# Performance work log

Measured on AMD Instinct MI355X. Metric: run time of the kernel, lower is better.

## Reference

```python
import jax, jax.numpy as jnp
import numpy as np

B, N, T, D, H, E = 2, 1024, 8, 128, 4, 8192
DH = D // H
NEG_SLOPE = 0.2  # GATv2Conv default negative_slope


def _ln(x, g, b):
    m = jnp.mean(x, -1, keepdims=True)
    v = jnp.mean((x - m) ** 2, -1, keepdims=True)
    return (x - m) * jax.lax.rsqrt(v + 1e-5) * g + b


def _forward(x, edge_index, gat_wl, gat_wr, gat_att, gat_b, in_w, in_b, out_w, out_b,
             ffn_w1, ffn_b1, ffn_w2, ffn_b2, fus_w, fus_b,
             lns_g, lns_b, lnt1_g, lnt1_b, lnt2_g, lnt2_b, lnf_g, lnf_b):
    # ---- spatial branch: GATv2, vectorized over (B, T) instead of python loops ----
    loops = jnp.arange(N)
    src = jnp.concatenate([edge_index[0], loops])  # j: message source (PyG adds self loops)
    dst = jnp.concatenate([edge_index[1], loops])  # i: aggregation target
    xl = jnp.einsum('bntd,de->bnte', x, gat_wl).reshape(B, N, T, H, D)
    xr = jnp.einsum('bntd,de->bnte', x, gat_wr).reshape(B, N, T, H, D)
    ml = xl[:, src]                                  # [B,Et,T,H,D]
    mr = xr[:, dst]
    e = jax.nn.leaky_relu(ml + mr, NEG_SLOPE)
    logits = jnp.einsum('bethd,hd->beth', e, gat_att)
    logits = jnp.moveaxis(logits, 1, 0)              # [Et,B,T,H]
    mx = jax.ops.segment_max(logits, dst, num_segments=N)
    p = jnp.exp(logits - mx[dst])                    # stable edge softmax per dst node
    ssum = jax.ops.segment_sum(p, dst, num_segments=N)
    alpha = p / ssum[dst]                            # [Et,B,T,H]
    msg = alpha[..., None] * jnp.moveaxis(ml, 1, 0)
    agg = jax.ops.segment_sum(msg, dst, num_segments=N)  # [N,B,T,H,D]
    x_sp = jnp.moveaxis(agg.mean(3), 0, 1) + gat_b   # concat=False -> head mean; [B,N,T,D]
    x_sp = _ln(x_sp, lns_g, lns_b)

    # ---- temporal branch: MHA + FFN, vectorized over all B*N nodes ----
    xt = x.reshape(B * N, T, D)
    qkv = xt @ in_w + in_b
    q, k, v = jnp.split(qkv, 3, axis=-1)
    q = q.reshape(B * N, T, H, DH)
    k = k.reshape(B * N, T, H, DH)
    v = v.reshape(B * N, T, H, DH)
    scores = jnp.einsum('bthd,bshd->bhts', q, k) / np.float32(np.sqrt(DH))
    attn = jax.nn.softmax(scores, -1)
    o = jnp.einsum('bhts,bshd->bthd', attn, v).reshape(B * N, T, D)
    o = o @ out_w + out_b
    x1 = _ln(xt + o, lnt1_g, lnt1_b)
    ffn = jax.nn.gelu(x1 @ ffn_w1 + ffn_b1, approximate=False) @ ffn_w2 + ffn_b2
    x_tp = _ln(x1 + ffn, lnt2_g, lnt2_b).reshape(B, N, T, D)

    # ---- gated fusion with residual ----
    g = jax.nn.sigmoid(jnp.concatenate([x_sp, x_tp], -1) @ fus_w + fus_b)
    return _ln(g * x_sp + (1.0 - g) * x_tp + x, lnf_g, lnf_b)


def setup_inputs() -> dict:
    key = jax.random.key(0)
    ks = jax.random.split(key, 12)
    s = 0.05
    f = jnp.float32
    return {
        'x': jax.random.normal(ks[0], (B, N, T, D), f),
        'edge_index': jax.random.randint(ks[1], (2, E), 0, N),
        'gat_wl': jax.random.normal(ks[2], (D, H * D), f) * s,
        'gat_wr': jax.random.normal(ks[3], (D, H * D), f) * s,
        'gat_att': jax.random.normal(ks[4], (H, D), f) * s,
        'gat_b': jnp.zeros((D,), f),
        'in_w': jax.random.normal(ks[5], (D, 3 * D), f) * s,
        'in_b': jnp.zeros((3 * D,), f),
        'out_w': jax.random.normal(ks[6], (D, D), f) * s,
        'out_b': jnp.zeros((D,), f),
        'ffn_w1': jax.random.normal(ks[7], (D, 4 * D), f) * s,
        'ffn_b1': jnp.zeros((4 * D,), f),
        'ffn_w2': jax.random.normal(ks[8], (4 * D, D), f) * s,
        'ffn_b2': jnp.zeros((D,), f),
        'fus_w': jax.random.normal(ks[9], (2 * D, D), f) * s,
        'fus_b': jnp.zeros((D,), f),
        'lns_g': jnp.ones((D,), f), 'lns_b': jnp.zeros((D,), f),
        'lnt1_g': jnp.ones((D,), f), 'lnt1_b': jnp.zeros((D,), f),
        'lnt2_g': jnp.ones((D,), f), 'lnt2_b': jnp.zeros((D,), f),
        'lnf_g': jnp.ones((D,), f), 'lnf_b': jnp.zeros((D,), f),
    }


def reference(x, edge_index, gat_wl, gat_wr, gat_att, gat_b, in_w, in_b, out_w, out_b,
              ffn_w1, ffn_b1, ffn_w2, ffn_b2, fus_w, fus_b,
              lns_g, lns_b, lnt1_g, lnt1_b, lnt2_g, lnt2_b, lnf_g, lnf_b):
    return _forward(x, edge_index, gat_wl, gat_wr, gat_att, gat_b, in_w, in_b, out_w, out_b,
                    ffn_w1, ffn_b1, ffn_w2, ffn_b2, fus_w, fus_b,
                    lns_g, lns_b, lnt1_g, lnt1_b, lnt2_g, lnt2_b, lnf_g, lnf_b)
```

## Files before the change

### kernel.cpp

```cpp
#include <hip/hip_runtime.h>
#include <math.h>

#define B_ 2
#define N_ 1024
#define T_ 8
#define D_ 128
#define H_ 4
#define E_ 8192
#define EN_ 9216
#define M_ 16384

typedef unsigned short u16;
using bf16x8 = __attribute__((ext_vector_type(8))) short;
using f32x4  = __attribute__((ext_vector_type(4))) float;

__device__ __forceinline__ float bf2f(unsigned int u) {
  return __uint_as_float(u << 16);
}
__device__ __forceinline__ u16 f2bf(float f) {
  unsigned int x = __float_as_uint(f);
  x += 0x7fffu + ((x >> 16) & 1u);
  return (u16)(x >> 16);
}
__device__ __forceinline__ void load8f(const u16* p, float* f) {
  uint4 u = *(const uint4*)p;
  f[0]=bf2f(u.x & 0xffffu); f[1]=bf2f(u.x >> 16);
  f[2]=bf2f(u.y & 0xffffu); f[3]=bf2f(u.y >> 16);
  f[4]=bf2f(u.z & 0xffffu); f[5]=bf2f(u.z >> 16);
  f[6]=bf2f(u.w & 0xffffu); f[7]=bf2f(u.w >> 16);
}
__device__ __forceinline__ void unpack8(uint4 u, float* f) {
  f[0]=bf2f(u.x & 0xffffu); f[1]=bf2f(u.x >> 16);
  f[2]=bf2f(u.y & 0xffffu); f[3]=bf2f(u.y >> 16);
  f[4]=bf2f(u.z & 0xffffu); f[5]=bf2f(u.z >> 16);
  f[6]=bf2f(u.w & 0xffffu); f[7]=bf2f(u.w >> 16);
}
__device__ __forceinline__ void gl2lds(const u16* g, u16* l) {
  __builtin_amdgcn_global_load_lds(
      (const __attribute__((address_space(1))) unsigned int*)(const void*)g,
      (__attribute__((address_space(3))) unsigned int*)(void*)l,
      16, 0, 0);
}

__device__ __forceinline__ size_t bt_row(int r) {
  return (size_t)(((r >> 13) << 3) | (r & 7)) * 1024 + ((r >> 3) & 1023);
}

__device__ __forceinline__ u16 conv_w_elem(int idx,
    const float* wl, const float* wr, const float* inw, const float* outw,
    const float* f1, const float* f2, const float* fw) {
  const float* src; int base, K, N;
  if      (idx < 65536)  { src = wl;   base = 0;      K = 128; N = 512; }
  else if (idx < 131072) { src = wr;   base = 65536;  K = 128; N = 512; }
  else if (idx < 180224) { src = inw;  base = 131072; K = 128; N = 384; }
  else if (idx < 196608) { src = outw; base = 180224; K = 128; N = 128; }
  else if (idx < 262144) { src = f1;   base = 196608; K = 128; N = 512; }
  else if (idx < 327680) { src = f2;   base = 262144; K = 512; N = 128; }
  else                   { src = fw;   base = 327680; K = 256; N = 128; }
  int o = idx - base;
  int n = o / K, k = o - n * K;
  return f2bf(src[k * N + n]);
}

__global__ __launch_bounds__(1024) void prep_csr_k(const float* __restrict__ x,
    const float* __restrict__ wl, const float* __restrict__ wr,
    const float* __restrict__ inw, const float* __restrict__ outw,
    const float* __restrict__ f1, const float* __restrict__ f2,
    const float* __restrict__ fw,
    u16* __restrict__ XB, u16* __restrict__ WB,
    const int* __restrict__ ei, int* __restrict__ offs, int* __restrict__ srcs) {
  __shared__ int cnt[N_];
  __shared__ int cur[N_];
  int bi = blockIdx.x;
  int tid = threadIdx.x;
  if (bi < 512) {
    int i = (bi * 1024 + tid) * 4;
    float4 v = *(const float4*)&x[i];
    u16 o[4] = {f2bf(v.x), f2bf(v.y), f2bf(v.z), f2bf(v.w)};
    *(ushort4*)&XB[i] = *(ushort4*)o;
    return;
  }
  if (bi < 600) {
    int base = (bi - 512) * 4096 + tid * 4;
#pragma unroll
    for (int j = 0; j < 4; ++j)
      WB[base + j] = conv_w_elem(base + j, wl, wr, inw, outw, f1, f2, fw);
    return;
  }
  cnt[tid] = 0;
  __syncthreads();
  for (int e = tid; e < EN_; e += 1024) {
    int d = (e < E_) ? ei[E_ + e] : (e - E_);
    atomicAdd(&cnt[d], 1);
  }
  __syncthreads();
  int mine = cnt[tid];
  for (int off = 1; off < 1024; off <<= 1) {
    int tv = (tid >= off) ? cnt[tid - off] : 0;
    __syncthreads();
    cnt[tid] += tv;
    __syncthreads();
  }
  int excl = cnt[tid] - mine;
  offs[tid] = excl;
  if (tid == 1023) offs[N_] = cnt[1023];
  cur[tid] = excl;
  __syncthreads();
  for (int e = tid; e < EN_; e += 1024) {
    int d = (e < E_) ? ei[E_ + e] : (e - E_);
    int s = (e < E_) ? ei[e] : (e - E_);
    int pos = atomicAdd(&cur[d], 1);
    srcs[pos] = s;
  }
}

__global__ __launch_bounds__(256) void proj_k(const u16* __restrict__ XB,
    const u16* __restrict__ WT1, const float* __restrict__ in_b,
    u16* __restrict__ XL, u16* __restrict__ XR, u16* __restrict__ QKV) {
  __shared__ u16 As[128 * 128];
  __shared__ u16 Bs[128 * 128];
  int bx = blockIdx.x, by = blockIdx.y;
  int tid = threadIdx.x;
  int lane = tid & 63, wid = tid >> 6;
  int lr = lane & 15, lk = lane >> 4;
  int wm = (wid >> 1) * 64, wn = (wid & 1) * 64;

#pragma unroll
  for (int kc = 0; kc < 4; ++kc) {
#pragma unroll
    for (int i = 0; i < 2; ++i) {
      int o = tid * 16 + i * 4096;
      int row = o >> 6;
      int col = (o >> 1) & 31;
      gl2lds(XB + (size_t)(by * 128 + row) * 128 + kc * 32 + col,
             (u16*)((char*)As + kc * 8192 + i * 4096 + wid * 1024));
      gl2lds(WT1 + (size_t)(bx * 128 + row) * 128 + kc * 32 + col,
             (u16*)((char*)Bs + kc * 8192 + i * 4096 + wid * 1024));
    }
  }
  __syncthreads();

  f32x4 acc[4][4] = {};
#pragma unroll
  for (int kc = 0; kc < 4; ++kc) {
    bf16x8 bf[4];
#pragma unroll
    for (int ni = 0; ni < 4; ++ni)
      bf[ni] = *(const bf16x8*)&Bs[kc * 4096 + (wn + ni * 16 + lr) * 32 + lk * 8];
#pragma unroll
    for (int mi = 0; mi < 4; ++mi) {
      bf16x8 af = *(const bf16x8*)&As[kc * 4096 + (wm + mi * 16 + lr) * 32 + lk * 8];
#pragma unroll
      for (int ni = 0; ni < 4; ++ni)
        acc[mi][ni] = __builtin_amdgcn_mfma_f32_16x16x32_bf16(af, bf[ni], acc[mi][ni], 0, 0, 0);
    }
  }

  u16* Cb; int ldc_; int col0; const float* bias_; int remap;
  if (bx < 4)      { Cb = XL;  ldc_ = 512; col0 = bx * 128;       bias_ = nullptr; remap = 1; }
  else if (bx < 8) { Cb = XR;  ldc_ = 512; col0 = (bx - 4) * 128; bias_ = nullptr; remap = 1; }
  else             { Cb = QKV; ldc_ = 384; col0 = (bx - 8) * 128; bias_ = in_b;    remap = 0; }
  float bc[4];
#pragma unroll
  for (int ni = 0; ni < 4; ++ni)
    bc[ni] = bias_ ? bias_[col0 + wn + ni * 16 + lr] : 0.f;

  __syncthreads();
#pragma unroll
  for (int mi = 0; mi < 4; ++mi) {
#pragma unroll
    for (int r = 0; r < 4; ++r) {
      int rowl = wm + mi * 16 + lk * 4 + r;
#pragma unroll
      for (int ni = 0; ni < 4; ++ni) {
        int col = wn + ni * 16 + lr;
        As[rowl * 128 + (col ^ ((rowl & 7) << 3))] = f2bf(acc[mi][ni][r] + bc[ni]);
      }
    }
  }
  __syncthreads();
  {
    int chunk = tid & 15;
    int rbase = tid >> 4;
#pragma unroll
    for (int pass = 0; pass < 8; ++pass) {
      int rowl = pass * 16 + rbase;
      int row = by * 128 + rowl;
      size_t orow = remap ? bt_row(row) : (size_t)row;
      int sw = (chunk ^ (rowl & 7)) * 8;
      *(uint4*)&Cb[orow * ldc_ + col0 + chunk * 8] =
          *(const uint4*)&As[rowl * 128 + sw];
    }
  }
}

__global__ __launch_bounds__(256) void gat_k(const u16* __restrict__ XL,
    const u16* __restrict__ XR,
    const int* __restrict__ offs, const int* __restrict__ srcs,
    const float* __restrict__ att, const float* __restrict__ gb,
    const float* __restrict__ lng, const float* __restrict__ lnb,
    u16* __restrict__ XCAT) {
  int bid = blockIdx.x;
  int lane = threadIdx.x & 63;
  int wid = threadIdx.x >> 6;
  int xcd = bid & 7;
  int slot = bid >> 3;
  int p = ((slot >> 8) << 3) | xcd;
  int n = (slot & 255) * 4 + wid;
  int b = p >> 3, t = p & 7;
  int dd = (lane & 15) * 8;
  size_t tokn = (size_t)(b * N_ + n) * 8 + t;
  const u16* XLs = XL + (size_t)p * 1024 * 512;

  float mr[8], av[8];
  load8f(XR + ((size_t)p * 1024 + n) * 512 + lane * 8, mr);
  *(float4*)&av[0] = *(const float4*)(att + lane * 8);
  *(float4*)&av[4] = *(const float4*)(att + lane * 8 + 4);

  int beg = offs[n], end = offs[n + 1];
  float sH = 0.f;
  float acc[8] = {0.f, 0.f, 0.f, 0.f, 0.f, 0.f, 0.f, 0.f};
  int i = beg;
  uint4 r0 = *(const uint4*)(XLs + (size_t)srcs[i] * 512 + lane * 8);
  uint4 r1 = r0;
  if (i + 1 < end)
    r1 = *(const uint4*)(XLs + (size_t)srcs[i + 1] * 512 + lane * 8);
  while (i + 1 < end) {
    uint4 c0 = r0, c1 = r1;
    if (i + 2 < end)
      r0 = *(const uint4*)(XLs + (size_t)srcs[i + 2] * 512 + lane * 8);
    if (i + 3 < end)
      r1 = *(const uint4*)(XLs + (size_t)srcs[i + 3] * 512 + lane * 8);
    float ml0[8], ml1[8];
    unpack8(c0, ml0);
    unpack8(c1, ml1);
    float d0 = 0.f, d1 = 0.f;
#pragma unroll
    for (int j = 0; j < 8; ++j) {
      float m0 = ml0[j] + mr[j];
      m0 = fmaxf(m0, 0.2f * m0);
      d0 += m0 * av[j];
      float m1 = ml1[j] + mr[j];
      m1 = fmaxf(m1, 0.2f * m1);
      d1 += m1 * av[j];
    }
    d0 += __shfl_xor(d0, 1, 64); d1 += __shfl_xor(d1, 1, 64);
    d0 += __shfl_xor(d0, 2, 64); d1 += __shfl_xor(d1, 2, 64);
    d0 += __shfl_xor(d0, 4, 64); d1 += __shfl_xor(d1, 4, 64);
    d0 += __shfl_xor(d0, 8, 64); d1 += __shfl_xor(d1, 8, 64);
    float p0 = __expf(d0), p1 = __expf(d1);
    sH += p0 + p1;
#pragma unroll
    for (int j = 0; j < 8; ++j) acc[j] += p0 * ml0[j] + p1 * ml1[j];
    i += 2;
  }
  if (i < end) {
    float ml0[8];
    unpack8(r0, ml0);
    float d0 = 0.f;
#pragma unroll
    for (int j = 0; j < 8; ++j) {
      float m0 = ml0[j] + mr[j];
      m0 = fmaxf(m0, 0.2f * m0);
      d0 += m0 * av[j];
    }
    d0 += __shfl_xor(d0, 1, 64);
    d0 += __shfl_xor(d0, 2, 64);
    d0 += __shfl_xor(d0, 4, 64);
    d0 += __shfl_xor(d0, 8, 64);
    float p0 = __expf(d0);
    sH += p0;
#pragma unroll
    for (int j = 0; j < 8; ++j) acc[j] += p0 * ml0[j];
  }
  float invS = 1.f / sH;
#pragma unroll
  for (int j = 0; j < 8; ++j) acc[j] *= invS;
#pragma unroll
  for (int j = 0; j < 8; ++j) {
    acc[j] += __shfl_xor(acc[j], 16, 64);
    acc[j] += __shfl_xor(acc[j], 32, 64);
  }
#pragma unroll
  for (int j = 0; j < 8; ++j) acc[j] = acc[j] * 0.25f + gb[dd + j];
  float s = 0.f, s2 = 0.f;
#pragma unroll
  for (int j = 0; j < 8; ++j) { s += acc[j]; s2 += acc[j] * acc[j]; }
#pragma unroll
  for (int m = 1; m < 16; m <<= 1) {
    s += __shfl_xor(s, m, 64);
    s2 += __shfl_xor(s2, m, 64);
  }
  float mean = s * (1.f / 128.f);
  float var = s2 * (1.f / 128.f) - mean * mean;
  float r = rsqrtf(var + 1e-5f);
  if (lane < 16) {
    u16 ob[8];
#pragma unroll
    for (int j = 0; j < 8; ++j)
      ob[j] = f2bf((acc[j] - mean) * r * lng[dd + j] + lnb[dd + j]);
    *(uint4*)&XCAT[tokn * 256 + dd] = *(uint4*)ob;
  }
}

__global__ __launch_bounds__(256) void tower_k(const u16* __restrict__ QKV,
    const u16* __restrict__ WTO, const float* __restrict__ out_b,
    const float* __restrict__ x,
    const float* __restrict__ lnt1_g, const float* __restrict__ lnt1_b,
    const u16* __restrict__ WTF1, const u16* __restrict__ WTF2,
    const float* __restrict__ b1, const float* __restrict__ b2,
    const float* __restrict__ lnt2_g, const float* __restrict__ lnt2_b,
    u16* __restrict__ XCATr) {
  __shared__ u16 P[4 * 32 * 32];
  __shared__ u16 Wb[16384];
  __shared__ u16 Hc[2 * 32 * 40];
  __shared__ float rs[64], rq[64];
  int by = blockIdx.x;
  int tid = threadIdx.x;
  int lane = tid & 63, wid = tid >> 6;
  int lr = lane & 15, lk = lane >> 4;
  int wm = (wid >> 1) * 16, wn = (wid & 1) * 64;

#pragma unroll
  for (int i = 0; i < 8; ++i) {
    int o = tid * 16 + i * 4096;
    int c = o >> 13;
    int wb = o & 8191;
    int nrow = wb >> 6;
    int kin = (wb & 63) >> 1;
    gl2lds(WTO + (size_t)nrow * 128 + c * 32 + kin,
           (u16*)((char*)Wb + wid * 1024 + i * 4096));
  }
  int t = lane >> 3, sidx = lane & 7, dg = lane & 7;
  for (int it = 0; it < 4; ++it) {
    int task = wid * 4 + it;
    int bnl = task >> 2, h = task & 3;
    int bn = by * 4 + bnl;
    const u16* base = QKV + (size_t)bn * 8 * 384;
    float va[8][4];
#pragma unroll
    for (int s2 = 0; s2 < 8; ++s2) {
      ushort4 vv = *(const ushort4*)(base + s2 * 384 + 256 + h * 32 + dg * 4);
      va[s2][0] = bf2f(vv.x); va[s2][1] = bf2f(vv.y);
      va[s2][2] = bf2f(vv.z); va[s2][3] = bf2f(vv.w);
    }
    const u16* qp = base + t * 384 + h * 32;
    const u16* kp = base + sidx * 384 + 128 + h * 32;
    float sc = 0.f;
#pragma unroll
    for (int d0 = 0; d0 < 32; d0 += 8) {
      float q[8], k[8];
      load8f(qp + d0, q);
      load8f(kp + d0, k);
#pragma unroll
      for (int j = 0; j < 8; ++j) sc += q[j] * k[j];
    }
    sc *= 0.17677669529663687f;
    float m = sc;
    m = fmaxf(m, __shfl_xor(m, 1, 64));
    m = fmaxf(m, __shfl_xor(m, 2, 64));
    m = fmaxf(m, __shfl_xor(m, 4, 64));
    float p = __expf(sc - m);
    float S = p;
    S += __shfl_xor(S, 1, 64);
    S += __shfl_xor(S, 2, 64);
    S += __shfl_xor(S, 4, 64);
    float alpha = p / S;
    int tb = lane & 56;
    float o0 = 0.f, o1 = 0.f, o2 = 0.f, o3 = 0.f;
#pragma unroll
    for (int s2 = 0; s2 < 8; ++s2) {
      float a = __shfl(alpha, tb + s2, 64);
      o0 += a * va[s2][0];
      o1 += a * va[s2][1];
      o2 += a * va[s2][2];
      o3 += a * va[s2][3];
    }
    u16 ov[4] = {f2bf(o0), f2bf(o1), f2bf(o2), f2bf(o3)};
    int row = bnl * 8 + t;
    *(ushort4*)&P[h * 1024 + row * 32 + dg * 4] = *(ushort4*)ov;
  }
  __syncthreads();

  f32x4 acc[4] = {};
#pragma unroll
  for (int c = 0; c < 4; ++c) {
    bf16x8 bf[4];
#pragma unroll
    for (int ni = 0; ni < 4; ++ni)
      bf[ni] = *(const bf16x8*)&Wb[c * 4096 + (wn + ni * 16 + lr) * 32 + lk * 8];
    bf16x8 af = *(const bf16x8*)&P[c * 1024 + (wm + lr) * 32 + lk * 8];
#pragma unroll
    for (int ni = 0; ni < 4; ++ni)
      acc[ni] = __builtin_amdgcn_mfma_f32_16x16x32_bf16(af, bf[ni], acc[ni], 0, 0, 0);
  }

  f32x4 x1r[4];
  {
    float bc[4];
#pragma unroll
    for (int ni = 0; ni < 4; ++ni) bc[ni] = out_b[wn + ni * 16 + lr];
#pragma unroll
    for (int r = 0; r < 4; ++r) {
      int rowl = wm + lk * 4 + r;
      int row = by * 32 + rowl;
      float s = 0.f, s2 = 0.f;
#pragma unroll
      for (int ni = 0; ni < 4; ++ni) {
        int col = wn + ni * 16 + lr;
        float v = acc[ni][r] + bc[ni] + x[(size_t)row * 128 + col];
        acc[ni][r] = v;
        s += v; s2 += v * v;
      }
      s += __shfl_xor(s, 1, 64); s2 += __shfl_xor(s2, 1, 64);
      s += __shfl_xor(s, 2, 64); s2 += __shfl_xor(s2, 2, 64);
      s += __shfl_xor(s, 4, 64); s2 += __shfl_xor(s2, 4, 64);
      s += __shfl_xor(s, 8, 64); s2 += __shfl_xor(s2, 8, 64);
      if (lr == 0) {
        rs[rowl * 2 + (wid & 1)] = s;
        rq[rowl * 2 + (wid & 1)] = s2;
      }
    }
    __syncthreads();
#pragma unroll
    for (int r = 0; r < 4; ++r) {
      int rowl = wm + lk * 4 + r;
      float tot = rs[rowl * 2] + rs[rowl * 2 + 1];
      float tq = rq[rowl * 2] + rq[rowl * 2 + 1];
      float mean = tot * (1.f / 128.f);
      float var = tq * (1.f / 128.f) - mean * mean;
      float rinv = rsqrtf(var + 1e-5f);
#pragma unroll
      for (int ni = 0; ni < 4; ++ni) {
        int col = wn + ni * 16 + lr;
        float o = (acc[ni][r] - mean) * rinv * lnt1_g[col] + lnt1_b[col];
        x1r[ni][r] = o;
        P[(col >> 5) * 1024 + rowl * 32 + (col & 31)] = f2bf(o);
      }
    }
  }

  int wr0 = (wid >> 1) * 16, wc0 = (wid & 1) * 32;
  f32x4 acc2[4] = {};
  for (int nc = 0; nc < 8; ++nc) {
    __syncthreads();
#pragma unroll
    for (int kc = 0; kc < 4; ++kc) {
      gl2lds(WTF1 + (size_t)(nc * 64 + (tid >> 2)) * 128 + kc * 32 + (tid & 3) * 8,
             (u16*)((char*)Wb + kc * 4096 + wid * 1024));
    }
#pragma unroll
    for (int i = 0; i < 4; ++i) {
      int o = tid * 16 + i * 4096;
      int kc2l = o >> 13;
      int wb = o & 8191;
      int nrow = wb >> 6;
      int kin = (wb & 63) >> 1;
      gl2lds(WTF2 + (size_t)nrow * 512 + nc * 64 + kc2l * 32 + kin,
             (u16*)((char*)Wb + 16384 + wid * 1024 + i * 4096));
    }
    __syncthreads();
    f32x4 a1[2] = {};
#pragma unroll
    for (int kc = 0; kc < 4; ++kc) {
      bf16x8 bf0 = *(const bf16x8*)&Wb[kc * 2048 + (wc0 + lr) * 32 + lk * 8];
      bf16x8 bf1 = *(const bf16x8*)&Wb[kc * 2048 + (wc0 + 16 + lr) * 32 + lk * 8];
      bf16x8 af = *(const bf16x8*)&P[kc * 1024 + (wr0 + lr) * 32 + lk * 8];
      a1[0] = __builtin_amdgcn_mfma_f32_16x16x32_bf16(af, bf0, a1[0], 0, 0, 0);
      a1[1] = __builtin_amdgcn_mfma_f32_16x16x32_bf16(af, bf1, a1[1], 0, 0, 0);
    }
#pragma unroll
    for (int r = 0; r < 4; ++r) {
      int row = wr0 + lk * 4 + r;
#pragma unroll
      for (int ni = 0; ni < 2; ++ni) {
        int cl = wc0 + ni * 16 + lr;
        float v = a1[ni][r] + b1[nc * 64 + cl];
        v = 0.5f * v * (1.f + erff(v * 0.70710678118f));
        Hc[(cl >> 5) * 1280 + row * 40 + (cl & 31)] = f2bf(v);
      }
    }
    __syncthreads();
#pragma unroll
    for (int kc2l = 0; kc2l < 2; ++kc2l) {
      bf16x8 bf[4];
#pragma unroll
      for (int ni = 0; ni < 4; ++ni)
        bf[ni] = *(const bf16x8*)&Wb[8192 + kc2l * 4096 + (wn + ni * 16 + lr) * 32 + lk * 8];
      bf16x8 af = *(const bf16x8*)&Hc[kc2l * 1280 + (wm + lr) * 40 + lk * 8];
#pragma unroll
      for (int ni = 0; ni < 4; ++ni)
        acc2[ni] = __builtin_amdgcn_mfma_f32_16x16x32_bf16(af, bf[ni], acc2[ni], 0, 0, 0);
    }
  }
  __syncthreads();

  {
    float bc[4];
#pragma unroll
    for (int ni = 0; ni < 4; ++ni) bc[ni] = b2[wn + ni * 16 + lr];
#pragma unroll
    for (int r = 0; r < 4; ++r) {
      int rowl = wm + lk * 4 + r;
      float s = 0.f, s2 = 0.f;
#pragma unroll
      for (int ni = 0; ni < 4; ++ni) {
        float v = acc2[ni][r] + bc[ni] + x1r[ni][r];
        acc2[ni][r] = v;
        s += v; s2 += v * v;
      }
      s += __shfl_xor(s, 1, 64); s2 += __shfl_xor(s2, 1, 64);
      s += __shfl_xor(s, 2, 64); s2 += __shfl_xor(s2, 2, 64);
      s += __shfl_xor(s, 4, 64); s2 += __shfl_xor(s2, 4, 64);
      s += __shfl_xor(s, 8, 64); s2 += __shfl_xor(s2, 8, 64);
      if (lr == 0) {
        rs[rowl * 2 + (wid & 1)] = s;
        rq[rowl * 2 + (wid & 1)] = s2;
      }
    }
    __syncthreads();
#pragma unroll
    for (int r = 0; r < 4; ++r) {
      int rowl = wm + lk * 4 + r;
      float tot = rs[rowl * 2] + rs[rowl * 2 + 1];
      float tq = rq[rowl * 2] + rq[rowl * 2 + 1];
      float mean = tot * (1.f / 128.f);
      float var = tq * (1.f / 128.f) - mean * mean;
      float rinv = rsqrtf(var + 1e-5f);
#pragma unroll
      for (int ni = 0; ni < 4; ++ni) {
        int col = wn + ni * 16 + lr;
        float o = (acc2[ni][r] - mean) * rinv * lnt2_g[col] + lnt2_b[col];
        P[rowl * 128 + (col ^ ((rowl & 7) << 3))] = f2bf(o);
      }
    }
    __syncthreads();
    {
      int chunk = tid & 15;
      int rbase = tid >> 4;
#pragma unroll
      for (int pass = 0; pass < 2; ++pass) {
        int rowl = pass * 16 + rbase;
        int sw = (chunk ^ (rowl & 7)) * 8;
        *(uint4*)&XCATr[(size_t)(by * 32 + rowl) * 256 + chunk * 8] =
            *(const uint4*)&P[rowl * 128 + sw];
      }
    }
  }
}

__global__ __launch_bounds__(256) void fusion_k(const u16* __restrict__ A,
    const u16* __restrict__ WT, const float* __restrict__ bias,
    const float* __restrict__ xres, const u16* __restrict__ xcat,
    const float* __restrict__ lng, const float* __restrict__ lnb,
    float* __restrict__ o32) {
  __shared__ u16 As[32 * 32];
  __shared__ u16 Bs[128 * 32];
  __shared__ float rs[64], rq[64];
  int by = blockIdx.x;
  int tid = threadIdx.x;
  int lane = tid & 63, wid = tid >> 6;
  int lr = lane & 15, lk = lane >> 4;
  int wm = (wid >> 1) * 16, wn = (wid & 1) * 64;
  const int K = 256;

  f32x4 acc[4] = {};
  for (int k0 = 0; k0 < K; k0 += 32) {
    __syncthreads();
    if (tid < 128) {
      int o = tid * 16;
      gl2lds(A + (size_t)(by * 32 + (o >> 6)) * K + k0 + ((o >> 1) & 31),
             (u16*)((char*)As + wid * 1024));
    }
#pragma unroll
    for (int i = 0; i < 2; ++i) {
      int o = tid * 16 + i * 4096;
      gl2lds(WT + (size_t)(o >> 6) * K + k0 + ((o >> 1) & 31),
             (u16*)((char*)Bs + wid * 1024 + i * 4096));
    }
    __syncthreads();
    bf16x8 bf[4];
#pragma unroll
    for (int ni = 0; ni < 4; ++ni)
      bf[ni] = *(const bf16x8*)&Bs[(wn + ni * 16 + lr) * 32 + lk * 8];
    bf16x8 af = *(const bf16x8*)&As[(wm + lr) * 32 + lk * 8];
#pragma unroll
    for (int ni = 0; ni < 4; ++ni)
      acc[ni] = __builtin_amdgcn_mfma_f32_16x16x32_bf16(af, bf[ni], acc[ni], 0, 0, 0);
  }
  float bc[4];
#pragma unroll
  for (int ni = 0; ni < 4; ++ni) bc[ni] = bias[wn + ni * 16 + lr];
#pragma unroll
  for (int r = 0; r < 4; ++r) {
    int rowl = wm + lk * 4 + r;
    int row = by * 32 + rowl;
    float s = 0.f, s2 = 0.f;
#pragma unroll
    for (int ni = 0; ni < 4; ++ni) {
      int col = wn + ni * 16 + lr;
      float v = acc[ni][r] + bc[ni];
      float gg = 1.f / (1.f + __expf(-v));
      float xsp = bf2f(xcat[(size_t)row * 256 + col]);
      float xtp = bf2f(xcat[(size_t)row * 256 + 128 + col]);
      v = gg * xsp + (1.f - gg) * xtp + xres[(size_t)row * 128 + col];
      acc[ni][r] = v;
      s += v; s2 += v * v;
    }
    s += __shfl_xor(s, 1, 64); s2 += __shfl_xor(s2, 1, 64);
    s += __shfl_xor(s, 2, 64); s2 += __shfl_xor(s2, 2, 64);
    s += __shfl_xor(s, 4, 64); s2 += __shfl_xor(s2, 4, 64);
    s += __shfl_xor(s, 8, 64); s2 += __shfl_xor(s2, 8, 64);
    if (lr == 0) {
      rs[rowl * 2 + (wid & 1)] = s;
      rq[rowl * 2 + (wid & 1)] = s2;
    }
  }
  __syncthreads();
#pragma unroll
  for (int r = 0; r < 4; ++r) {
    int rowl = wm + lk * 4 + r;
    int row = by * 32 + rowl;
    float tot = rs[rowl * 2] + rs[rowl * 2 + 1];
    float tq = rq[rowl * 2] + rq[rowl * 2 + 1];
    float mean = tot * (1.f / 128.f);
    float var = tq * (1.f / 128.f) - mean * mean;
    float rinv = rsqrtf(var + 1e-5f);
#pragma unroll
    for (int ni = 0; ni < 4; ++ni) {
      int col = wn + ni * 16 + lr;
      o32[(size_t)row * 128 + col] =
          (acc[ni][r] - mean) * rinv * lng[col] + lnb[col];
    }
  }
}

extern "C" void kernel_launch(void* const* d_in, const int* in_sizes, int n_in,
                              void* d_out, int out_size, void* d_ws, size_t ws_size,
                              hipStream_t stream) {
  const float* x       = (const float*)d_in[0];
  const int*   ei      = (const int*)d_in[1];
  const float* gat_att = (const float*)d_in[4];
  const float* gat_b   = (const float*)d_in[5];
  const float* in_b    = (const float*)d_in[7];
  const float* out_b   = (const float*)d_in[9];
  const float* ffn_b1  = (const float*)d_in[11];
  const float* ffn_b2  = (const float*)d_in[13];
  const float* fus_b   = (const float*)d_in[15];
  const float* lns_g   = (const float*)d_in[16];
  const float* lns_b   = (const float*)d_in[17];
  const float* lnt1_g  = (const float*)d_in[18];
  const float* lnt1_b  = (const float*)d_in[19];
  const float* lnt2_g  = (const float*)d_in[20];
  const float* lnt2_b  = (const float*)d_in[21];
  const float* lnf_g   = (const float*)d_in[22];
  const float* lnf_b   = (const float*)d_in[23];

  char* ws = (char*)d_ws;
  u16*   WB    = (u16*)ws;
  u16*   WTO   = WB + 180224;
  u16*   WTF1  = WB + 196608;
  u16*   WTF2  = WB + 262144;
  u16*   WTFUS = WB + 327680;
  int*   OFFS  = (int*)(ws + 3145728);
  int*   SRCS  = (int*)(ws + 3153920);
  u16*   XB   = (u16*)(ws + 4194304);
  u16*   XL   = (u16*)(ws + 8388608);
  u16*   XR   = (u16*)(ws + 25165824);
  u16*   QKV  = (u16*)(ws + 50331648);
  u16*   XCAT = (u16*)(ws + 67108864);

  prep_csr_k<<<dim3(601), dim3(1024), 0, stream>>>(x,
      (const float*)d_in[2], (const float*)d_in[3], (const float*)d_in[6],
      (const float*)d_in[8], (const float*)d_in[10], (const float*)d_in[12],
      (const float*)d_in[14], XB, WB, ei, OFFS, SRCS);

  proj_k<<<dim3(11, 128), dim3(256), 0, stream>>>(XB, WB, in_b, XL, XR, QKV);

  gat_k<<<dim3(4096), dim3(256), 0, stream>>>(XL, XR, OFFS, SRCS,
      gat_att, gat_b, lns_g, lns_b, XCAT);

  tower_k<<<dim3(512), dim3(256), 0, stream>>>(QKV, WTO, out_b, x,
      lnt1_g, lnt1_b, WTF1, WTF2, ffn_b1, ffn_b2, lnt2_g, lnt2_b, XCAT + 128);

  fusion_k<<<dim3(512), dim3(256), 0, stream>>>(XCAT, WTFUS, fus_b, x, XCAT,
      lnf_g, lnf_b, (float*)d_out);
}
```

Baseline: 201.0 us.

## Fuse gated fusion GEMM and final LayerNorm into the temporal tower kernel

New measurement: 200.1 us. About the same (-0.4%).

```diff
diff --git a/kernel.cpp b/kernel.cpp
--- a/kernel.cpp
+++ b/kernel.cpp
@@ -199,7 +199,7 @@
     const int* __restrict__ offs, const int* __restrict__ srcs,
     const float* __restrict__ att, const float* __restrict__ gb,
     const float* __restrict__ lng, const float* __restrict__ lnb,
-    u16* __restrict__ XCAT) {
+    u16* __restrict__ XSP) {
   int bid = blockIdx.x;
   int lane = threadIdx.x & 63;
   int wid = threadIdx.x >> 6;
@@ -299,7 +299,7 @@
 #pragma unroll
     for (int j = 0; j < 8; ++j)
       ob[j] = f2bf((acc[j] - mean) * r * lng[dd + j] + lnb[dd + j]);
-    *(uint4*)&XCAT[tokn * 256 + dd] = *(uint4*)ob;
+    *(uint4*)&XSP[tokn * 128 + dd] = *(uint4*)ob;
   }
 }
 
@@ -310,10 +310,12 @@
     const u16* __restrict__ WTF1, const u16* __restrict__ WTF2,
     const float* __restrict__ b1, const float* __restrict__ b2,
     const float* __restrict__ lnt2_g, const float* __restrict__ lnt2_b,
-    u16* __restrict__ XCATr) {
-  __shared__ u16 P[4 * 32 * 32];
+    const u16* __restrict__ WTFUS, const float* __restrict__ fus_b,
+    const float* __restrict__ lnf_g, const float* __restrict__ lnf_b,
+    const u16* __restrict__ XSP, float* __restrict__ o32) {
+  __shared__ u16 P[32 * 128];
   __shared__ u16 Wb[16384];
-  __shared__ u16 Hc[2 * 32 * 40];
+  __shared__ u16 Hc[4096];
   __shared__ float rs[64], rq[64];
   int by = blockIdx.x;
   int tid = threadIdx.x;
@@ -495,6 +497,27 @@
   }
   __syncthreads();
 
+#pragma unroll
+  for (int i = 0; i < 8; ++i) {
+    int o = tid * 16 + i * 4096;
+    int rl = o >> 6;
+    int kcf = rl >> 7;
+    int nrow = rl & 127;
+    int kin = (o & 63) >> 1;
+    gl2lds(WTFUS + (size_t)nrow * 256 + kcf * 32 + kin,
+           (u16*)((char*)Wb + wid * 1024 + i * 4096));
+  }
+#pragma unroll
+  for (int i = 0; i < 2; ++i) {
+    int o = tid * 16 + i * 4096;
+    int rl = o >> 6;
+    int kcf = rl >> 5;
+    int rowl = rl & 31;
+    int kin = (o & 63) >> 1;
+    gl2lds(XSP + (size_t)(by * 32 + rowl) * 128 + kcf * 32 + kin,
+           (u16*)((char*)Hc + wid * 1024 + i * 4096));
+  }
+
   {
     float bc[4];
 #pragma unroll
@@ -531,106 +554,94 @@
       for (int ni = 0; ni < 4; ++ni) {
         int col = wn + ni * 16 + lr;
         float o = (acc2[ni][r] - mean) * rinv * lnt2_g[col] + lnt2_b[col];
+        acc2[ni][r] = o;
         P[rowl * 128 + (col ^ ((rowl & 7) << 3))] = f2bf(o);
       }
     }
-    __syncthreads();
-    {
-      int chunk = tid & 15;
-      int rbase = tid >> 4;
-#pragma unroll
-      for (int pass = 0; pass < 2; ++pass) {
-        int rowl = pass * 16 + rbase;
-        int sw = (chunk ^ (rowl & 7)) * 8;
-        *(uint4*)&XCATr[(size_t)(by * 32 + rowl) * 256 + chunk * 8] =
-            *(const uint4*)&P[rowl * 128 + sw];
-      }
-    }
-  }
-}
-
-__global__ __launch_bounds__(256) void fusion_k(const u16* __restrict__ A,
-    const u16* __restrict__ WT, const float* __restrict__ bias,
-    const float* __restrict__ xres, const u16* __restrict__ xcat,
-    const float* __restrict__ lng, const float* __restrict__ lnb,
-    float* __restrict__ o32) {
-  __shared__ u16 As[32 * 32];
-  __shared__ u16 Bs[128 * 32];
-  __shared__ float rs[64], rq[64];
-  int by = blockIdx.x;
-  int tid = threadIdx.x;
-  int lane = tid & 63, wid = tid >> 6;
-  int lr = lane & 15, lk = lane >> 4;
-  int wm = (wid >> 1) * 16, wn = (wid & 1) * 64;
-  const int K = 256;
-
-  f32x4 acc[4] = {};
-  for (int k0 = 0; k0 < K; k0 += 32) {
-    __syncthreads();
-    if (tid < 128) {
-      int o = tid * 16;
-      gl2lds(A + (size_t)(by * 32 + (o >> 6)) * K + k0 + ((o >> 1) & 31),
-             (u16*)((char*)As + wid * 1024));
-    }
-#pragma unroll
-    for (int i = 0; i < 2; ++i) {
-      int o = tid * 16 + i * 4096;
-      gl2lds(WT + (size_t)(o >> 6) * K + k0 + ((o >> 1) & 31),
-             (u16*)((char*)Bs + wid * 1024 + i * 4096));
-    }
-    __syncthreads();
+  }
+  __syncthreads();
+
+  f32x4 acc3[4] = {};
+#pragma unroll
+  for (int kc = 0; kc < 4; ++kc) {
     bf16x8 bf[4];
 #pragma unroll
     for (int ni = 0; ni < 4; ++ni)
-      bf[ni] = *(const bf16x8*)&Bs[(wn + ni * 16 + lr) * 32 + lk * 8];
-    bf16x8 af = *(const bf16x8*)&As[(wm + lr) * 32 + lk * 8];
+      bf[ni] = *(const bf16x8*)&Wb[kc * 4096 + (wn + ni * 16 + lr) * 32 + lk * 8];
+    bf16x8 af = *(const bf16x8*)&Hc[kc * 1024 + (wm + lr) * 32 + lk * 8];
 #pragma unroll
     for (int ni = 0; ni < 4; ++ni)
-      acc[ni] = __builtin_amdgcn_mfma_f32_16x16x32_bf16(af, bf[ni], acc[ni], 0, 0, 0);
-  }
-  float bc[4];
-#pragma unroll
-  for (int ni = 0; ni < 4; ++ni) bc[ni] = bias[wn + ni * 16 + lr];
-#pragma unroll
-  for (int r = 0; r < 4; ++r) {
-    int rowl = wm + lk * 4 + r;
-    int row = by * 32 + rowl;
-    float s = 0.f, s2 = 0.f;
-#pragma unroll
-    for (int ni = 0; ni < 4; ++ni) {
-      int col = wn + ni * 16 + lr;
-      float v = acc[ni][r] + bc[ni];
-      float gg = 1.f / (1.f + __expf(-v));
-      float xsp = bf2f(xcat[(size_t)row * 256 + col]);
-      float xtp = bf2f(xcat[(size_t)row * 256 + 128 + col]);
-      v = gg * xsp + (1.f - gg) * xtp + xres[(size_t)row * 128 + col];
-      acc[ni][r] = v;
-      s += v; s2 += v * v;
-    }
-    s += __shfl_xor(s, 1, 64); s2 += __shfl_xor(s2, 1, 64);
-    s += __shfl_xor(s, 2, 64); s2 += __shfl_xor(s2, 2, 64);
-    s += __shfl_xor(s, 4, 64); s2 += __shfl_xor(s2, 4, 64);
-    s += __shfl_xor(s, 8, 64); s2 += __shfl_xor(s2, 8, 64);
-    if (lr == 0) {
-      rs[rowl * 2 + (wid & 1)] = s;
-      rq[rowl * 2 + (wid & 1)] = s2;
-    }
-  }
-  __syncthreads();
-#pragma unroll
-  for (int r = 0; r < 4; ++r) {
-    int rowl = wm + lk * 4 + r;
-    int row = by * 32 + rowl;
-    float tot = rs[rowl * 2] + rs[rowl * 2 + 1];
-    float tq = rq[rowl * 2] + rq[rowl * 2 + 1];
-    float mean = tot * (1.f / 128.f);
-    float var = tq * (1.f / 128.f) - mean * mean;
-    float rinv = rsqrtf(var + 1e-5f);
-#pragma unroll
-    for (int ni = 0; ni < 4; ++ni) {
-      int col = wn + ni * 16 + lr;
-      o32[(size_t)row * 128 + col] =
-          (acc[ni][r] - mean) * rinv * lng[col] + lnb[col];
+      acc3[ni] = __builtin_amdgcn_mfma_f32_16x16x32_bf16(af, bf[ni], acc3[ni], 0, 0, 0);
+  }
+  __syncthreads();
+#pragma unroll
+  for (int i = 0; i < 8; ++i) {
+    int o = tid * 16 + i * 4096;
+    int rl = o >> 6;
+    int kcf = rl >> 7;
+    int nrow = rl & 127;
+    int kin = (o & 63) >> 1;
+    gl2lds(WTFUS + (size_t)nrow * 256 + 128 + kcf * 32 + kin,
+           (u16*)((char*)Wb + wid * 1024 + i * 4096));
+  }
+  __syncthreads();
+#pragma unroll
+  for (int kc = 0; kc < 4; ++kc) {
+    bf16x8 bf[4];
+#pragma unroll
+    for (int ni = 0; ni < 4; ++ni)
+      bf[ni] = *(const bf16x8*)&Wb[kc * 4096 + (wn + ni * 16 + lr) * 32 + lk * 8];
+    int arow = wm + lr;
+    bf16x8 af = *(const bf16x8*)&P[arow * 128 + ((kc * 32 + lk * 8) ^ ((arow & 7) << 3))];
+#pragma unroll
+    for (int ni = 0; ni < 4; ++ni)
+      acc3[ni] = __builtin_amdgcn_mfma_f32_16x16x32_bf16(af, bf[ni], acc3[ni], 0, 0, 0);
+  }
+  {
+    float bc[4];
+#pragma unroll
+    for (int ni = 0; ni < 4; ++ni) bc[ni] = fus_b[wn + ni * 16 + lr];
+#pragma unroll
+    for (int r = 0; r < 4; ++r) {
+      int rowl = wm + lk * 4 + r;
+      int row = by * 32 + rowl;
+      float s = 0.f, s2 = 0.f;
+#pragma unroll
+      for (int ni = 0; ni < 4; ++ni) {
+        int col = wn + ni * 16 + lr;
+        float v = acc3[ni][r] + bc[ni];
+        float gg = 1.f / (1.f + __expf(-v));
+        float xsp = bf2f((unsigned int)Hc[(col >> 5) * 1024 + rowl * 32 + (col & 31)]);
+        float xtp = acc2[ni][r];
+        v = gg * xsp + (1.f - gg) * xtp + x[(size_t)row * 128 + col];
+        acc3[ni][r] = v;
+        s += v; s2 += v * v;
+      }
+      s += __shfl_xor(s, 1, 64); s2 += __shfl_xor(s2, 1, 64);
+      s += __shfl_xor(s, 2, 64); s2 += __shfl_xor(s2, 2, 64);
+      s += __shfl_xor(s, 4, 64); s2 += __shfl_xor(s2, 4, 64);
+      s += __shfl_xor(s, 8, 64); s2 += __shfl_xor(s2, 8, 64);
+      if (lr == 0) {
+        rs[rowl * 2 + (wid & 1)] = s;
+        rq[rowl * 2 + (wid & 1)] = s2;
+      }
+    }
+    __syncthreads();
+#pragma unroll
+    for (int r = 0; r < 4; ++r) {
+      int rowl = wm + lk * 4 + r;
+      int row = by * 32 + rowl;
+      float tot = rs[rowl * 2] + rs[rowl * 2 + 1];
+      float tq = rq[rowl * 2] + rq[rowl * 2 + 1];
+      float mean = tot * (1.f / 128.f);
+      float var = tq * (1.f / 128.f) - mean * mean;
+      float rinv = rsqrtf(var + 1e-5f);
+#pragma unroll
+      for (int ni = 0; ni < 4; ++ni) {
+        int col = wn + ni * 16 + lr;
+        o32[(size_t)row * 128 + col] =
+            (acc3[ni][r] - mean) * rinv * lnf_g[col] + lnf_b[col];
+      }
     }
   }
 }
@@ -668,7 +679,7 @@
   u16*   XL   = (u16*)(ws + 8388608);
   u16*   XR   = (u16*)(ws + 25165824);
   u16*   QKV  = (u16*)(ws + 50331648);
-  u16*   XCAT = (u16*)(ws + 67108864);
+  u16*   XSP  = (u16*)(ws + 67108864);
 
   prep_csr_k<<<dim3(601), dim3(1024), 0, stream>>>(x,
       (const float*)d_in[2], (const float*)d_in[3], (const float*)d_in[6],
@@ -678,11 +689,9 @@
   proj_k<<<dim3(11, 128), dim3(256), 0, stream>>>(XB, WB, in_b, XL, XR, QKV);
 
   gat_k<<<dim3(4096), dim3(256), 0, stream>>>(XL, XR, OFFS, SRCS,
-      gat_att, gat_b, lns_g, lns_b, XCAT);
+      gat_att, gat_b, lns_g, lns_b, XSP);
 
   tower_k<<<dim3(512), dim3(256), 0, stream>>>(QKV, WTO, out_b, x,
-      lnt1_g, lnt1_b, WTF1, WTF2, ffn_b1, ffn_b2, lnt2_g, lnt2_b, XCAT + 128);
-
-  fusion_k<<<dim3(512), dim3(256), 0, stream>>>(XCAT, WTFUS, fus_b, x, XCAT,
-      lnf_g, lnf_b, (float*)d_out);
-}
+      lnt1_g, lnt1_b, WTF1, WTF2, ffn_b1, ffn_b2, lnt2_g, lnt2_b,
+      WTFUS, fus_b, lnf_g, lnf_b, XSP, (float*)d_out);
+}
```
